# Optimization experiments

Measured on AMD Instinct MI355X. Metric: run time of the kernel, lower is better.

Reference implementation:

```python
import jax, jax.numpy as jnp
import numpy as np

N, E, F_IN, F_HID, F_OUT = 50000, 800000, 128, 128, 64


def setup_inputs() -> dict:
    key = jax.random.key(0)
    k_x, k_e, k_w1, k_w2 = jax.random.split(key, 4)
    x = jax.random.normal(k_x, (N, F_IN), dtype=jnp.float32)
    edge_index = jax.random.randint(k_e, (2, E), 0, N, dtype=jnp.int32)
    # GCNConv params (glorot-ish scale)
    W1 = jax.random.normal(k_w1, (F_IN, F_HID), dtype=jnp.float32) * (1.0 / np.sqrt(F_IN))
    b1 = jnp.zeros((F_HID,), dtype=jnp.float32)
    W2 = jax.random.normal(k_w2, (F_HID, F_OUT), dtype=jnp.float32) * (1.0 / np.sqrt(F_HID))
    b2 = jnp.zeros((F_OUT,), dtype=jnp.float32)
    return {"x": x, "edge_index": edge_index, "W1": W1, "b1": b1, "W2": W2, "b2": b2}


def reference(x, edge_index, W1, b1, W2, b2):
    n = x.shape[0]
    # PyG GCNConv: add self-loops, symmetric normalization deg^-1/2 * deg^-1/2
    loops = jnp.arange(n, dtype=edge_index.dtype)
    src = jnp.concatenate([edge_index[0], loops])  # (E+N,)
    dst = jnp.concatenate([edge_index[1], loops])  # (E+N,)
    deg = jax.ops.segment_sum(jnp.ones_like(dst, dtype=x.dtype), dst, num_segments=n)
    dinv = jnp.where(deg > 0, jax.lax.rsqrt(jnp.maximum(deg, 1.0)), 0.0)
    norm = dinv[src] * dinv[dst]  # (E+N,)

    def conv(h, W, b):
        h = h @ W                               # (n, f_out)
        msg = h[src] * norm[:, None]            # gather + scale, (E+N, f_out)
        return jax.ops.segment_sum(msg, dst, num_segments=n) + b

    h = jax.nn.relu(conv(x, W1, b1))  # dropout p=0.0 -> identity
    return conv(h, W2, b2)
```

## Files before the change

kernel.cpp:

```cpp
#include <hip/hip_runtime.h>

typedef __bf16 bf16x8 __attribute__((ext_vector_type(8)));
typedef float  f32x4  __attribute__((ext_vector_type(4)));
typedef int    i32x4  __attribute__((ext_vector_type(4)));
typedef unsigned int u32x4 __attribute__((ext_vector_type(4)));

#define NTLOAD(p)    __builtin_nontemporal_load(p)

__device__ __forceinline__ float bf2f(unsigned short h) {
    return __uint_as_float(((unsigned int)h) << 16);
}
__device__ __forceinline__ unsigned short f2bf(float f) {
    unsigned int u = __float_as_uint(f);
    u += 0x7FFFu + ((u >> 16) & 1u);
    return (unsigned short)(u >> 16);
}
__device__ __forceinline__ void unpack8(u32x4 u, float* v) {
#pragma unroll
    for (int k = 0; k < 4; ++k) {
        v[2 * k]     = __uint_as_float(u[k] << 16);
        v[2 * k + 1] = __uint_as_float(u[k] & 0xFFFF0000u);
    }
}

__device__ __forceinline__ int detect_cnt(const unsigned short* __restrict__ x,
                                          int* sc, int t) {
    int c = 0;
    for (int i = t; i < 4096; i += 256) {
        unsigned e = (x[i] >> 7) & 0xFFu;
        if (e >= 0x88u) ++c;
    }
    sc[t] = c;
    __syncthreads();
    for (int d = 128; d > 0; d >>= 1) {
        if (t < d) sc[t] += sc[t + d];
        __syncthreads();
    }
    return sc[0];
}

template <int COLS>
__device__ __forceinline__ void prepack_one(const void* W, unsigned short* Wp, int idx,
                                            bool isf32) {
    if (idx >= (COLS / 16) * 4 * 64) return;
    int lane = idx & 63;
    int ks   = (idx >> 6) & 3;
    int nt   = idx >> 8;
    int col  = nt * 16 + (lane & 15);
    int krow = ks * 32 + (lane >> 4) * 8;
    unsigned short tmp[8];
#pragma unroll
    for (int j = 0; j < 8; ++j) {
        size_t e = (size_t)(krow + j) * COLS + col;
        float v = isf32 ? ((const float*)W)[e] : bf2f(((const unsigned short*)W)[e]);
        tmp[j] = f2bf(v);
    }
    *(u32x4*)(Wp + (size_t)idx * 8) = *(u32x4*)tmp;
}

__global__ void k0_prep(const unsigned short* __restrict__ x, int* __restrict__ dflag,
                        int* __restrict__ cnt, int N,
                        const void* __restrict__ W1, const void* __restrict__ W2,
                        const void* __restrict__ b1, const void* __restrict__ b2,
                        unsigned short* __restrict__ Wp1, unsigned short* __restrict__ Wp2,
                        float* __restrict__ b1f, float* __restrict__ b2f) {
    __shared__ int sc[256];
    int t = threadIdx.x;
    int bid = (int)blockIdx.x;
    if (bid < 13) {
        int c = detect_cnt(x, sc, t);
        bool isf32 = (c >= 16);
        if (bid < 8) {
            prepack_one<128>(W1, Wp1, bid * 256 + t, isf32);
        } else if (bid < 12) {
            prepack_one<64>(W2, Wp2, (bid - 8) * 256 + t, isf32);
        } else {
            if (t == 0) dflag[0] = c;
            if (t < 128) b1f[t] = isf32 ? ((const float*)b1)[t]
                                        : bf2f(((const unsigned short*)b1)[t]);
            else if (t < 192) b2f[t - 128] = isf32 ? ((const float*)b2)[t - 128]
                                                   : bf2f(((const unsigned short*)b2)[t - 128]);
        }
    } else {
        int i = (bid - 13) * 1024 + t * 4;
        if (i + 4 <= N) *(i32x4*)(cnt + i) = (i32x4){0, 0, 0, 0};
        else for (int k = i; k < N; ++k) cnt[k] = 0;
    }
}

__device__ __forceinline__ void gemm1_body(const void* __restrict__ X,
                                           const unsigned short* __restrict__ Wp,
                                           unsigned short* __restrict__ O, int nstrips,
                                           bool xf32, int blockI,
                                           unsigned short* __restrict__ Ls) {
    constexpr int NT = 8;
    const int wave = threadIdx.x >> 6;
    const int lane = threadIdx.x & 63;
    const int strip = blockI * 4 + wave;
    const bool active = (strip < nstrips);
    const int m = lane & 15;
    const int q = lane >> 4;
    unsigned short* lw = Ls + wave * (16 * 136);

    if (active) {
        const unsigned rowoff = (unsigned)(strip * 16 + m) * 128u + (unsigned)(q * 8);
        f32x4 acc[NT];
#pragma unroll
        for (int nt = 0; nt < NT; ++nt) acc[nt] = (f32x4){0.f, 0.f, 0.f, 0.f};

#pragma unroll
        for (int ks = 0; ks < 4; ++ks) {
            bf16x8 a;
            if (xf32) {
                const float* xp = (const float*)X + rowoff + ks * 32;
                f32x4 u = NTLOAD((f32x4*)xp);
                f32x4 v = NTLOAD((f32x4*)xp + 1);
                unsigned short tmp[8];
                tmp[0] = f2bf(u[0]); tmp[1] = f2bf(u[1]);
                tmp[2] = f2bf(u[2]); tmp[3] = f2bf(u[3]);
                tmp[4] = f2bf(v[0]); tmp[5] = f2bf(v[1]);
                tmp[6] = f2bf(v[2]); tmp[7] = f2bf(v[3]);
                a = *(bf16x8*)tmp;
            } else {
                a = NTLOAD((bf16x8*)((const unsigned short*)X + rowoff + ks * 32));
            }
#pragma unroll
            for (int nt = 0; nt < NT; ++nt) {
                bf16x8 b = *(const bf16x8*)(Wp + (unsigned)(((nt * 4 + ks) * 64 + lane) * 8));
                acc[nt] = __builtin_amdgcn_mfma_f32_16x16x32_bf16(a, b, acc[nt], 0, 0, 0);
            }
        }

#pragma unroll
        for (int nt = 0; nt < NT; ++nt) {
#pragma unroll
            for (int r = 0; r < 4; ++r)
                lw[(q * 4 + r) * 136 + nt * 16 + m] = f2bf(acc[nt][r]);
        }
    }

    __syncthreads();

    if (active) {
        const int r0 = strip * 16;
#pragma unroll
        for (int i = 0; i < 4; ++i) {
            int c = lane + 64 * i;
            int row = c >> 4, k = c & 15;
            u32x4 v = *(const u32x4*)&lw[row * 136 + k * 8];
            *(u32x4*)(O + (unsigned)(r0 + row) * 128u + (unsigned)(k * 8)) = v;
        }
    }
}

__global__ __launch_bounds__(256) void k1_scatter_gemm1(
        const int* __restrict__ src, const int* __restrict__ dst,
        int* __restrict__ cnt, int* __restrict__ adj, int E, int SB,
        const void* __restrict__ X, const unsigned short* __restrict__ Wp1,
        unsigned short* __restrict__ Hb, int nstrips, const int* __restrict__ dflag) {
    __shared__ unsigned short Ls[4 * 16 * 136];
    if ((int)blockIdx.x < SB) {
        int e0 = (blockIdx.x * 256 + threadIdx.x) * 8;
        if (e0 + 8 <= E) {
            i32x4 d0 = NTLOAD((i32x4*)(dst + e0));
            i32x4 d1 = NTLOAD((i32x4*)(dst + e0 + 4));
            i32x4 s0 = NTLOAD((i32x4*)(src + e0));
            i32x4 s1 = NTLOAD((i32x4*)(src + e0 + 4));
#pragma unroll
            for (int k = 0; k < 4; ++k) {
                int p = atomicAdd(&cnt[d0[k]], 1);
                if (p < 64) adj[((unsigned)d0[k] << 6) + p] = s0[k];
            }
#pragma unroll
            for (int k = 0; k < 4; ++k) {
                int p = atomicAdd(&cnt[d1[k]], 1);
                if (p < 64) adj[((unsigned)d1[k] << 6) + p] = s1[k];
            }
        } else {
            for (int e = e0; e < E; ++e) {
                int d = dst[e];
                int p = atomicAdd(&cnt[d], 1);
                if (p < 64) adj[((unsigned)d << 6) + p] = src[e];
            }
        }
    } else {
        gemm1_body(X, Wp1, Hb, nstrips, (*dflag >= 16), blockIdx.x - SB, Ls);
    }
}

__global__ void k2_dinv(const int* __restrict__ cnt, float* __restrict__ dinv, int N) {
    int i = blockIdx.x * 1024 + threadIdx.x * 4;
    if (i + 4 <= N) {
        i32x4 c = *(const i32x4*)(cnt + i);
        f32x4 d;
#pragma unroll
        for (int k = 0; k < 4; ++k) d[k] = rsqrtf((float)c[k] + 1.0f);
        *(f32x4*)(dinv + i) = d;
    } else {
        for (int k = i; k < N; ++k) dinv[k] = rsqrtf((float)cnt[k] + 1.0f);
    }
}

__global__ __launch_bounds__(256) void gather1_gemm2(
        const unsigned short* __restrict__ Hb, const float* __restrict__ dinv,
        const int* __restrict__ cnt, const float* __restrict__ b,
        const int* __restrict__ adj, const unsigned short* __restrict__ Wp2,
        unsigned short* __restrict__ H2b, int N) {
    __shared__ unsigned short Rs[16][136];
    __shared__ unsigned short Hs[16][72];
    const int strip = blockIdx.x;
    const int tid = threadIdx.x;
    const int lane = tid & 63;

    {
        int ndl = tid >> 4;
        int nd = strip * 16 + ndl;
        int l15 = lane & 15;
        int gbase = lane & ~15;
        unsigned f8 = (unsigned)(l15 * 8);
        if (nd < N) {
            float acc[8];
#pragma unroll
            for (int k = 0; k < 8; ++k) acc[k] = 0.f;
            int len = min(cnt[nd], 64);
            const int* arow = adj + ((unsigned)nd << 6);
            for (int c = 0; c < len; c += 16) {
                int rem = len - c;
                int myadj = (l15 < rem) ? NTLOAD((int*)&arow[c + l15]) : 0;
                float myw = (l15 < rem) ? dinv[myadj] : 0.f;
#pragma unroll
                for (int t = 0; t < 16; t += 8) {
                    if (t >= rem) break;
                    int sI[8];
#pragma unroll
                    for (int k = 0; k < 8; ++k) sI[k] = __shfl(myadj, gbase + t + k, 64);
                    u32x4 u[8];
#pragma unroll
                    for (int k = 0; k < 8; ++k)
                        u[k] = *(const u32x4*)(Hb + ((unsigned)sI[k] << 7) + f8);
                    float n[8];
#pragma unroll
                    for (int k = 0; k < 8; ++k) n[k] = __shfl(myw, gbase + t + k, 64);
#pragma unroll
                    for (int k = 0; k < 8; ++k) {
                        float v[8];
                        unpack8(u[k], v);
#pragma unroll
                        for (int j = 0; j < 8; ++j) acc[j] = fmaf(v[j], n[k], acc[j]);
                    }
                }
            }
            float dd = dinv[nd];
            float hv[8], bb[8];
            unpack8(*(const u32x4*)(Hb + ((unsigned)nd << 7) + f8), hv);
            *(f32x4*)&bb[0] = *(const f32x4*)(b + f8);
            *(f32x4*)&bb[4] = *(const f32x4*)(b + f8 + 4);
            unsigned short o[8];
#pragma unroll
            for (int k = 0; k < 8; ++k) {
                float a = fmaf(fmaf(hv[k], dd, acc[k]), dd, bb[k]);
                o[k] = f2bf(fmaxf(a, 0.f));
            }
            *(u32x4*)&Rs[ndl][f8] = *(u32x4*)o;
        } else {
            *(u32x4*)&Rs[ndl][f8] = (u32x4){0u, 0u, 0u, 0u};
        }
    }
    __syncthreads();

    {
        const int nt = tid >> 6;
        const int m = lane & 15;
        const int q = lane >> 4;
        f32x4 acc = (f32x4){0.f, 0.f, 0.f, 0.f};
#pragma unroll
        for (int ks = 0; ks < 4; ++ks) {
            bf16x8 a = *(const bf16x8*)&Rs[m][ks * 32 + q * 8];
            bf16x8 bfr = *(const bf16x8*)(Wp2 + (unsigned)(((nt * 4 + ks) * 64 + lane) * 8));
            acc = __builtin_amdgcn_mfma_f32_16x16x32_bf16(a, bfr, acc, 0, 0, 0);
        }
        const int rr = strip * 16 + q * 4;
        f32x4 dv;
        if (rr + 3 < N) {
            dv = *(const f32x4*)(dinv + rr);
        } else {
#pragma unroll
            for (int r = 0; r < 4; ++r) dv[r] = (rr + r < N) ? dinv[rr + r] : 0.f;
        }
#pragma unroll
        for (int r = 0; r < 4; ++r)
            Hs[q * 4 + r][nt * 16 + m] = f2bf(acc[r] * dv[r]);
    }
    __syncthreads();
    if (tid < 128) {
        int row = tid >> 3, k = tid & 7;
        int grow = strip * 16 + row;
        if (grow < N) {
            u32x4 v = *(const u32x4*)&Hs[row][k * 8];
            *(u32x4*)(H2b + (unsigned)grow * 64u + (unsigned)(k * 8)) = v;
        }
    }
}

__global__ void gather2(const unsigned short* __restrict__ H2b, const float* __restrict__ dinv,
                        const int* __restrict__ cnt, const float* __restrict__ b,
                        const int* __restrict__ adj, void* __restrict__ out,
                        int N, const int* __restrict__ dflag) {
    bool isf32 = (*dflag >= 16);
    int nd = blockIdx.x * 32 + (threadIdx.x >> 3);
    int lane = threadIdx.x & 63;
    int l7 = lane & 7;
    int gbase = lane & ~7;
    unsigned f8 = (unsigned)(l7 * 8);
    if (nd >= N) return;

    float acc[8];
#pragma unroll
    for (int k = 0; k < 8; ++k) acc[k] = 0.f;

    int len = min(cnt[nd], 64);
    const int* arow = adj + ((unsigned)nd << 6);
    for (int c = 0; c < len; c += 8) {
        int rem = len - c;
        int myadj = (l7 < rem) ? NTLOAD((int*)&arow[c + l7]) : 0;
        int sI[8];
#pragma unroll
        for (int k = 0; k < 8; ++k) sI[k] = __shfl(myadj, gbase + k, 64);
        u32x4 u[8];
#pragma unroll
        for (int k = 0; k < 8; ++k)
            u[k] = *(const u32x4*)(H2b + ((unsigned)sI[k] << 6) + f8);
        float n[8];
#pragma unroll
        for (int k = 0; k < 8; ++k) n[k] = (k < rem) ? 1.f : 0.f;
#pragma unroll
        for (int k = 0; k < 8; ++k) {
            float v[8];
            unpack8(u[k], v);
#pragma unroll
            for (int j = 0; j < 8; ++j) acc[j] = fmaf(v[j], n[k], acc[j]);
        }
    }
    float dd = dinv[nd];
    float hv[8], bb[8];
    unpack8(*(const u32x4*)(H2b + ((unsigned)nd << 6) + f8), hv);
    *(f32x4*)&bb[0] = *(const f32x4*)(b + f8);
    *(f32x4*)&bb[4] = *(const f32x4*)(b + f8 + 4);
    float r[8];
#pragma unroll
    for (int k = 0; k < 8; ++k) r[k] = fmaf(acc[k] + hv[k], dd, bb[k]);
    if (isf32) {
        float* op = (float*)out + (unsigned)nd * 64u + f8;
        *(f32x4*)op       = *(f32x4*)&r[0];
        *(f32x4*)(op + 4) = *(f32x4*)&r[4];
    } else {
        unsigned short o[8];
#pragma unroll
        for (int k = 0; k < 8; ++k) o[k] = f2bf(r[k]);
        *(u32x4*)((unsigned short*)out + (unsigned)nd * 64u + f8) = *(u32x4*)o;
    }
}

extern "C" void kernel_launch(void* const* d_in, const int* in_sizes, int n_in,
                              void* d_out, int out_size, void* d_ws, size_t ws_size,
                              hipStream_t stream) {
    const void* x  = d_in[0];
    const int*  ei = (const int*)d_in[1];
    const void* W1 = d_in[2];
    const void* b1 = d_in[3];
    const void* W2 = d_in[4];
    const void* b2 = d_in[5];

    const int N = in_sizes[0] / 128;
    const int E = in_sizes[1] / 2;
    const int* src = ei;
    const int* dst = ei + E;

    float* ws = (float*)d_ws;
    size_t off = 0;
    auto alloc = [&](size_t n) { size_t p = off; off += (n + 15) & ~(size_t)15; return p; };
    int*   dflag  = (int*)(ws + alloc(64));
    int*   cnt    = (int*)(ws + alloc(N));
    float* dinv   = ws + alloc(N);
    int*   adj    = (int*)(ws + alloc((size_t)N * 64));
    unsigned short* Hb  = (unsigned short*)(ws + alloc((size_t)N * 64));
    unsigned short* Wp1 = (unsigned short*)(ws + alloc(8192));
    unsigned short* Wp2 = (unsigned short*)(ws + alloc(4096));
    float* b1f    = ws + alloc(128);
    float* b2f    = ws + alloc(64);
    unsigned short* H2b = (unsigned short*)(ws + alloc((size_t)N * 32));

    const int EB8 = (E + 2047) / 2048;
    const int ZB  = (N + 1023) / 1024;
    const int nstrips = (N + 15) / 16;
    const int GB = (nstrips + 3) / 4;
    const int NB32 = (N + 31) / 32;

    k0_prep<<<13 + ZB, 256, 0, stream>>>((const unsigned short*)x, dflag, cnt, N,
                                         W1, W2, b1, b2, Wp1, Wp2, b1f, b2f);
    k1_scatter_gemm1<<<EB8 + GB, 256, 0, stream>>>(src, dst, cnt, adj, E, EB8,
                                                   x, Wp1, Hb, nstrips, dflag);
    k2_dinv<<<ZB, 256, 0, stream>>>(cnt, dinv, N);
    gather1_gemm2<<<nstrips, 256, 0, stream>>>(Hb, dinv, cnt, b1f, adj, Wp2, H2b, N);
    gather2<<<NB32, 256, 0, stream>>>(H2b, dinv, cnt, b2f, adj, d_out, N, dflag);
}
```

Before: 188.6 us.

## Partition edge scatter into eight destination ranges per edge chunk

The edge scatter launches eight blocks per 2048-edge chunk. Each block handles only destinations falling in one eighth of the node range, so the atomics and adjacency writes from each block land in a narrower address window, which should improve cache locality and may reduce contention. Every chunk's edge indices are now read eight times, and the nontemporal loads are replaced with normal cached loads, including the X loads in the GEMM part, so the repeated edge reads can hit in cache. The cost is eight times as many scatter blocks and redundant index traffic.

```diff
diff --git a/kernel.cpp b/kernel.cpp
--- a/kernel.cpp
+++ b/kernel.cpp
@@ -113,8 +113,8 @@
             bf16x8 a;
             if (xf32) {
                 const float* xp = (const float*)X + rowoff + ks * 32;
-                f32x4 u = NTLOAD((f32x4*)xp);
-                f32x4 v = NTLOAD((f32x4*)xp + 1);
+                f32x4 u = *(const f32x4*)xp;
+                f32x4 v = *((const f32x4*)xp + 1);
                 unsigned short tmp[8];
                 tmp[0] = f2bf(u[0]); tmp[1] = f2bf(u[1]);
                 tmp[2] = f2bf(u[2]); tmp[3] = f2bf(u[3]);
@@ -122,7 +122,7 @@
                 tmp[6] = f2bf(v[2]); tmp[7] = f2bf(v[3]);
                 a = *(bf16x8*)tmp;
             } else {
-                a = NTLOAD((bf16x8*)((const unsigned short*)X + rowoff + ks * 32));
+                a = *(const bf16x8*)((const unsigned short*)X + rowoff + ks * 32);
             }
 #pragma unroll
             for (int nt = 0; nt < NT; ++nt) {
@@ -155,32 +155,44 @@
 
 __global__ __launch_bounds__(256) void k1_scatter_gemm1(
         const int* __restrict__ src, const int* __restrict__ dst,
-        int* __restrict__ cnt, int* __restrict__ adj, int E, int SB,
+        int* __restrict__ cnt, int* __restrict__ adj, int E, int N, int SB,
         const void* __restrict__ X, const unsigned short* __restrict__ Wp1,
         unsigned short* __restrict__ Hb, int nstrips, const int* __restrict__ dflag) {
     __shared__ unsigned short Ls[4 * 16 * 136];
     if ((int)blockIdx.x < SB) {
-        int e0 = (blockIdx.x * 256 + threadIdx.x) * 8;
+        int sb = (int)blockIdx.x;
+        int chunk = sb >> 3;
+        int g = sb & 7;
+        int part = (N + 7) >> 3;
+        int lo = g * part;
+        int hi = min(lo + part, N);
+        int e0 = (chunk * 256 + threadIdx.x) * 8;
         if (e0 + 8 <= E) {
-            i32x4 d0 = NTLOAD((i32x4*)(dst + e0));
-            i32x4 d1 = NTLOAD((i32x4*)(dst + e0 + 4));
-            i32x4 s0 = NTLOAD((i32x4*)(src + e0));
-            i32x4 s1 = NTLOAD((i32x4*)(src + e0 + 4));
+            i32x4 d0 = *(const i32x4*)(dst + e0);
+            i32x4 d1 = *(const i32x4*)(dst + e0 + 4);
+            i32x4 s0 = *(const i32x4*)(src + e0);
+            i32x4 s1 = *(const i32x4*)(src + e0 + 4);
 #pragma unroll
             for (int k = 0; k < 4; ++k) {
-                int p = atomicAdd(&cnt[d0[k]], 1);
-                if (p < 64) adj[((unsigned)d0[k] << 6) + p] = s0[k];
+                if (d0[k] >= lo && d0[k] < hi) {
+                    int p = atomicAdd(&cnt[d0[k]], 1);
+                    if (p < 64) adj[((unsigned)d0[k] << 6) + p] = s0[k];
+                }
             }
 #pragma unroll
             for (int k = 0; k < 4; ++k) {
-                int p = atomicAdd(&cnt[d1[k]], 1);
-                if (p < 64) adj[((unsigned)d1[k] << 6) + p] = s1[k];
+                if (d1[k] >= lo && d1[k] < hi) {
+                    int p = atomicAdd(&cnt[d1[k]], 1);
+                    if (p < 64) adj[((unsigned)d1[k] << 6) + p] = s1[k];
+                }
             }
         } else {
             for (int e = e0; e < E; ++e) {
                 int d = dst[e];
-                int p = atomicAdd(&cnt[d], 1);
-                if (p < 64) adj[((unsigned)d << 6) + p] = src[e];
+                if (d >= lo && d < hi) {
+                    int p = atomicAdd(&cnt[d], 1);
+                    if (p < 64) adj[((unsigned)d << 6) + p] = src[e];
+                }
             }
         }
     } else {
@@ -391,6 +403,7 @@
     unsigned short* H2b = (unsigned short*)(ws + alloc((size_t)N * 32));
 
     const int EB8 = (E + 2047) / 2048;
+    const int SB  = EB8 * 8;
     const int ZB  = (N + 1023) / 1024;
     const int nstrips = (N + 15) / 16;
     const int GB = (nstrips + 3) / 4;
@@ -398,8 +411,8 @@
 
     k0_prep<<<13 + ZB, 256, 0, stream>>>((const unsigned short*)x, dflag, cnt, N,
                                          W1, W2, b1, b2, Wp1, Wp2, b1f, b2f);
-    k1_scatter_gemm1<<<EB8 + GB, 256, 0, stream>>>(src, dst, cnt, adj, E, EB8,
-                                                   x, Wp1, Hb, nstrips, dflag);
+    k1_scatter_gemm1<<<SB + GB, 256, 0, stream>>>(src, dst, cnt, adj, E, N, SB,
+                                                  x, Wp1, Hb, nstrips, dflag);
     k2_dinv<<<ZB, 256, 0, stream>>>(cnt, dinv, N);
     gather1_gemm2<<<nstrips, 256, 0, stream>>>(Hb, dinv, cnt, b1f, adj, Wp2, H2b, N);
     gather2<<<NB32, 256, 0, stream>>>(H2b, dinv, cnt, b2f, adj, d_out, N, dflag);
```

After: 183.6 us. 2.7% less time.
